# Kernel tuning notes

Measured on AMD Instinct MI355X. Metric: run time of the kernel, lower is better.

The kernel has to match this reference:

```python
import jax, jax.numpy as jnp
import numpy as np

L, D, H, FF = 4, 512, 8, 1024
B, S = 8, 480
TPT = 15          # TOKENS_PER_TURN
FIELD_IDX = 0
CAP = 6.0         # tanh logit soft cap
NEG = -1e30


def _layer_norm(x, g, b, eps=1e-5):
    m = jnp.mean(x, axis=-1, keepdims=True)
    v = jnp.mean((x - m) ** 2, axis=-1, keepdims=True)
    return (x - m) * jax.lax.rsqrt(v + eps) * g + b


def _episodic_mask(expanded_ids, n_prev_fields):
    # pokemon_batched_episodic_mask, vectorized -> [B, S, S] bool
    idx = jnp.arange(S)
    q_t = (idx // TPT)[:, None]            # [S,1]
    kv_t = (idx // TPT)[None, :]           # [1,S]
    kv_i = (idx % TPT)[None, :]
    same_turn = q_t == kv_t
    prev_field = (kv_i == FIELD_IDX) & (kv_t < q_t) & (q_t - kv_t <= n_prev_fields)
    same_ep = expanded_ids[:, :, None] == expanded_ids[:, None, :]  # [B,S,S]
    return same_ep & (same_turn | prev_field)[None]


def setup_inputs() -> dict:
    key = jax.random.key(0)
    ks = jax.random.split(key, 6)
    x = jax.random.normal(ks[0], (B, S, D), dtype=jnp.float32)
    expanded_ids = jnp.sort(jax.random.randint(ks[1], (B, S), 0, 3), axis=-1)
    inp = {
        "x": x,
        "expanded_ids": expanded_ids,
        "n_prev_fields": 8,
        "Wqkv": 0.02 * jax.random.normal(ks[2], (L, D, 3 * D), dtype=jnp.float32),
        "bqkv": jnp.zeros((L, 3 * D), jnp.float32),
        "Wo": 0.02 * jax.random.normal(ks[3], (L, D, D), dtype=jnp.float32),
        "bo": jnp.zeros((L, D), jnp.float32),
        "g1": jnp.ones((L, D), jnp.float32),
        "b1": jnp.zeros((L, D), jnp.float32),
        "g2": jnp.ones((L, D), jnp.float32),
        "b2": jnp.zeros((L, D), jnp.float32),
        "W1": 0.02 * jax.random.normal(ks[4], (L, D, FF), dtype=jnp.float32),
        "bf1": jnp.zeros((L, FF), jnp.float32),
        "W2": 0.02 * jax.random.normal(ks[5], (L, FF, D), dtype=jnp.float32),
        "bf2": jnp.zeros((L, D), jnp.float32),
    }
    return inp


def _encoder_layer(x, mask, Wqkv, bqkv, Wo, bo, g1, b1, g2, b2, W1, bf1, W2, bf2):
    hd = D // H
    h = _layer_norm(x, g1, b1)
    qkv = h @ Wqkv + bqkv                               # [B,S,3D]
    qkv = qkv.reshape(B, S, 3, H, hd)
    q, k, v = (qkv[:, :, i].transpose(0, 2, 1, 3) for i in range(3))  # [B,H,S,hd]
    scores = jnp.einsum("bhqd,bhkd->bhqk", q, k) / jnp.sqrt(jnp.float32(hd))
    scores = CAP * jnp.tanh(scores / CAP)               # logit soft cap (score_mod)
    scores = jnp.where(mask[:, None], scores, NEG)      # episodic block mask
    attn = jax.nn.softmax(scores, axis=-1)
    out = jnp.einsum("bhqk,bhkd->bhqd", attn, v)
    out = out.transpose(0, 2, 1, 3).reshape(B, S, D)
    x = x + (out @ Wo + bo)
    h2 = _layer_norm(x, g2, b2)
    ff = jax.nn.gelu(h2 @ W1 + bf1, approximate=False) @ W2 + bf2
    return x + ff


def reference(x, expanded_ids, n_prev_fields, Wqkv, bqkv, Wo, bo, g1, b1, g2, b2, W1, bf1, W2, bf2):
    mask = _episodic_mask(expanded_ids, n_prev_fields)
    for l in range(L):
        x = _encoder_layer(x, mask, Wqkv[l], bqkv[l], Wo[l], bo[l],
                           g1[l], b1[l], g2[l], b2[l], W1[l], bf1[l], W2[l], bf2[l])
    return x
```

## Files before the change

kernel.cpp:

```cpp
#include <hip/hip_runtime.h>
#include <hip/hip_bf16.h>
#include <hip/hip_fp16.h>
#include <math.h>

#define NL 4
#define Dm 512
#define Hh 8
#define FFD 1024
#define Bb 8
#define Ss 480
#define TPT 15
#define ROWS (Bb*Ss)

typedef __attribute__((ext_vector_type(8))) short short8v;
typedef __attribute__((ext_vector_type(4))) float f32x4;
typedef __attribute__((ext_vector_type(2))) _Float16 half2v;
typedef __attribute__((ext_vector_type(8))) _Float16 half8v;

#if __has_builtin(__builtin_amdgcn_fdot2)
#define FDOT2(a, b, c) __builtin_amdgcn_fdot2(a, b, c, false)
#else
#define FDOT2(a, b, c) ((c) + (float)(a)[0] * (float)(b)[0] + (float)(a)[1] * (float)(b)[1])
#endif

__device__ __forceinline__ void gld_lds16(const void* g, void* lbase, int lane) {
#if __has_builtin(__builtin_amdgcn_global_load_lds)
    __builtin_amdgcn_global_load_lds((const __attribute__((address_space(1))) void*)g,
                                     (__attribute__((address_space(3))) void*)lbase, 16, 0, 0);
#else
    *(short8v*)((char*)lbase + lane * 16) = *(const short8v*)g;
#endif
}

__global__ __launch_bounds__(256) void ln_kernel(const float* __restrict__ x,
                                                 const float* __restrict__ g,
                                                 const float* __restrict__ b,
                                                 __hip_bfloat16* __restrict__ out) {
    int row = blockIdx.x;
    const float* xr = x + (size_t)row * Dm;
    int tid = threadIdx.x;
    int wid = tid >> 6, lane = tid & 63;
    float v0 = xr[tid], v1 = xr[tid + 256];

    __shared__ float red[8];
    float s = v0 + v1;
    for (int off = 32; off; off >>= 1) s += __shfl_down(s, off);
    if (lane == 0) red[wid] = s;
    __syncthreads();
    if (tid == 0) red[0] = (red[0] + red[1] + red[2] + red[3]) * (1.0f / Dm);
    __syncthreads();
    float mean = red[0];

    float d0 = v0 - mean, d1 = v1 - mean;
    float ss = d0 * d0 + d1 * d1;
    for (int off = 32; off; off >>= 1) ss += __shfl_down(ss, off);
    if (lane == 0) red[4 + wid] = ss;
    __syncthreads();
    if (tid == 0) red[4] = (red[4] + red[5] + red[6] + red[7]) * (1.0f / Dm);
    __syncthreads();
    float rstd = rsqrtf(red[4] + 1e-5f);

    out[(size_t)row * Dm + tid]       = __float2bfloat16(d0 * rstd * g[tid]       + b[tid]);
    out[(size_t)row * Dm + tid + 256] = __float2bfloat16(d1 * rstd * g[tid + 256] + b[tid + 256]);
}

__global__ __launch_bounds__(256) void conv_t_kernel(const float* __restrict__ in,
                                                     __hip_bfloat16* __restrict__ out,
                                                     int K, int N) {
    const float* inz = in + (size_t)blockIdx.z * K * N;
    __hip_bfloat16* outz = out + (size_t)blockIdx.z * K * N;
    __shared__ float t[32][33];
    int n0 = blockIdx.x * 32, k0 = blockIdx.y * 32;
    int tx = threadIdx.x & 31, ty = threadIdx.x >> 5;
#pragma unroll
    for (int r = 0; r < 4; r++)
        t[ty * 4 + r][tx] = inz[(size_t)(k0 + ty * 4 + r) * N + n0 + tx];
    __syncthreads();
#pragma unroll
    for (int r = 0; r < 4; r++)
        outz[(size_t)(n0 + ty * 4 + r) * K + k0 + tx] = __float2bfloat16(t[tx][ty * 4 + r]);
}

template <int ACT, int RES, int OUTMODE>
__global__ __launch_bounds__(256) void gemm_mfma(const __hip_bfloat16* __restrict__ A,
                                                 const __hip_bfloat16* __restrict__ Bt,
                                                 const float* __restrict__ bias,
                                                 const float* __restrict__ res,
                                                 void* __restrict__ C,
                                                 int M, int N, int K) {
    __shared__ __align__(16) short As[64 * 64];
    __shared__ __align__(16) short Bs[64 * 64];
    const int bm = blockIdx.y * 64, bn = blockIdx.x * 64;
    const int tid = threadIdx.x;
    const int w = tid >> 6, lane = tid & 63;
    const int wm = (w >> 1) * 32, wn = (w & 1) * 32;
    const int l16 = lane & 15, lq = lane >> 4;
    const short* Ag = (const short*)A;
    const short* Bg = (const short*)Bt;

    f32x4 acc[2][2] = {};

    for (int k0 = 0; k0 < K; k0 += 64) {
#pragma unroll
        for (int r = 0; r < 2; ++r) {
            int row = r * 32 + w * 8 + (lane >> 3);
            int csrc = (lane & 7) ^ (row & 7);
            void* la = &As[(size_t)(r * 4096 + w * 1024) / 2];
            void* lb = &Bs[(size_t)(r * 4096 + w * 1024) / 2];
            gld_lds16(Ag + (size_t)(bm + row) * K + k0 + csrc * 8, la, lane);
            gld_lds16(Bg + (size_t)(bn + row) * K + k0 + csrc * 8, lb, lane);
        }
        __syncthreads();
#pragma unroll
        for (int kc = 0; kc < 2; ++kc) {
            short8v af[2], bf[2];
#pragma unroll
            for (int i = 0; i < 2; i++) {
                int row = wm + i * 16 + l16;
                int ch = (kc * 4 + lq) ^ (row & 7);
                af[i] = *(const short8v*)(&As[row * 64 + ch * 8]);
                int col = wn + i * 16 + l16;
                int ch2 = (kc * 4 + lq) ^ (col & 7);
                bf[i] = *(const short8v*)(&Bs[col * 64 + ch2 * 8]);
            }
#pragma unroll
            for (int i = 0; i < 2; i++)
#pragma unroll
                for (int j = 0; j < 2; j++)
                    acc[i][j] = __builtin_amdgcn_mfma_f32_16x16x32_bf16(
                        af[i], bf[j], acc[i][j], 0, 0, 0);
        }
        __syncthreads();
    }

#pragma unroll
    for (int i = 0; i < 2; i++) {
#pragma unroll
        for (int j = 0; j < 2; j++) {
#pragma unroll
            for (int r = 0; r < 4; r++) {
                int mrow = bm + wm + i * 16 + lq * 4 + r;
                int ncol = bn + wn + j * 16 + l16;
                float v = acc[i][j][r] + bias[ncol];
                if (ACT == 1) v = 0.5f * v * (1.0f + erff(v * 0.70710678118f));
                if (RES) v += res[(size_t)mrow * N + ncol];
                if (OUTMODE == 0)      ((float*)C)[(size_t)mrow * N + ncol] = v;
                else if (OUTMODE == 1) ((__hip_bfloat16*)C)[(size_t)mrow * N + ncol] = __float2bfloat16(v);
                else                   ((__half*)C)[(size_t)mrow * N + ncol] = __float2half(v);
            }
        }
    }
}

__global__ __launch_bounds__(256) void attn_sparse(const _Float16* __restrict__ qkv,
                                                   const int* __restrict__ ids,
                                                   const int* __restrict__ npf_p,
                                                   __hip_bfloat16* __restrict__ outb) {
    __shared__ _Float16 qs[4][512];
    __shared__ float ps[4][Hh][24];
    int w = threadIdx.x >> 6, lane = threadIdx.x & 63;
    int bq = blockIdx.x * 4 + w;
    int q = bq % Ss, b = bq / Ss;
    int npf = npf_p[0];
    int qt = q / TPT;
    int qid = ids[bq];

    *(half8v*)&qs[w][lane * 8] = *(const half8v*)&qkv[(size_t)bq * 1536 + lane * 8];
    __syncthreads();

    int h = lane >> 3, cp = lane & 7;

    half2v qreg[32];
#pragma unroll
    for (int i = 0; i < 32; i++) qreg[i] = *(const half2v*)&qs[w][h * 64 + i * 2];

    float s[3];
#pragma unroll
    for (int i = 0; i < 3; i++) {
        int c = cp + i * 8;
        float sv = -INFINITY;
        if (c < 23) {
            bool ok; int k;
            if (c < 15) { k = qt * TPT + c; ok = true; }
            else { int dt = c - 14; int kt = qt - dt; k = kt * TPT; ok = (kt >= 0) && (dt <= npf); }
            if (ok && ids[b * Ss + k] == qid) {
                const half8v* kr = (const half8v*)&qkv[(size_t)(b * Ss + k) * 1536 + 512 + h * 64];
                float dot = 0.0f;
#pragma unroll
                for (int cch = 0; cch < 8; cch++) {
                    half8v kv = kr[cch];
#pragma unroll
                    for (int e = 0; e < 4; e++) {
                        half2v kk = { kv[e * 2], kv[e * 2 + 1] };
                        dot = FDOT2(qreg[cch * 4 + e], kk, dot);
                    }
                }
                sv = 6.0f * tanhf(dot * (0.125f / 6.0f));
            }
        }
        s[i] = sv;
    }

    float m = fmaxf(fmaxf(s[0], s[1]), s[2]);
    for (int off = 1; off < 8; off <<= 1) m = fmaxf(m, __shfl_xor(m, off));
    float p0 = expf(s[0] - m), p1 = expf(s[1] - m), p2 = expf(s[2] - m);
    float l = p0 + p1 + p2;
    for (int off = 1; off < 8; off <<= 1) l += __shfl_xor(l, off);
    float inv = 1.0f / l;
    if (cp < 8)       ps[w][h][cp]      = p0 * inv;
    if (cp + 8 < 23)  ps[w][h][cp + 8]  = p1 * inv;
    if (cp + 16 < 23) ps[w][h][cp + 16] = p2 * inv;
    __syncthreads();

    int dg = lane & 7;
    float o[8] = {};
    for (int c = 0; c < 23; c++) {
        float p = ps[w][h][c];
        if (p != 0.0f) {
            int k = (c < 15) ? (qt * TPT + c) : ((qt - (c - 14)) * TPT);
            half8v vv = *(const half8v*)&qkv[(size_t)(b * Ss + k) * 1536 + 1024 + h * 64 + dg * 8];
#pragma unroll
            for (int e = 0; e < 8; e++) o[e] += p * (float)vv[e];
        }
    }
    short8v pack;
#pragma unroll
    for (int e = 0; e < 8; e++) {
        __hip_bfloat16 t = __float2bfloat16(o[e]);
        pack[e] = __builtin_bit_cast(short, t);
    }
    *(short8v*)&outb[(size_t)bq * Dm + h * 64 + dg * 8] = pack;
}

extern "C" void kernel_launch(void* const* d_in, const int* in_sizes, int n_in,
                              void* d_out, int out_size, void* d_ws, size_t ws_size,
                              hipStream_t stream) {
    const float* x    = (const float*)d_in[0];
    const int*   ids  = (const int*)d_in[1];
    const int*   npf  = (const int*)d_in[2];
    const float* Wqkv = (const float*)d_in[3];
    const float* bqkv = (const float*)d_in[4];
    const float* Wo   = (const float*)d_in[5];
    const float* bo   = (const float*)d_in[6];
    const float* g1   = (const float*)d_in[7];
    const float* b1   = (const float*)d_in[8];
    const float* g2   = (const float*)d_in[9];
    const float* b2   = (const float*)d_in[10];
    const float* W1   = (const float*)d_in[11];
    const float* bf1  = (const float*)d_in[12];
    const float* W2   = (const float*)d_in[13];
    const float* bf2  = (const float*)d_in[14];
    float* out = (float*)d_out;

    char* p = (char*)d_ws;
    __hip_bfloat16* hb    = (__hip_bfloat16*)p;   p += (size_t)ROWS * Dm * 2;
    _Float16*       qkvb  = (_Float16*)p;         p += (size_t)ROWS * 3 * Dm * 2;
    __hip_bfloat16* attnb = (__hip_bfloat16*)p;   p += (size_t)ROWS * Dm * 2;
    __hip_bfloat16* fb    = (__hip_bfloat16*)p;   p += (size_t)ROWS * FFD * 2;
    __hip_bfloat16* Wqkv_t= (__hip_bfloat16*)p;   p += (size_t)NL * Dm * 3 * Dm * 2;
    __hip_bfloat16* Wo_t  = (__hip_bfloat16*)p;   p += (size_t)NL * Dm * Dm * 2;
    __hip_bfloat16* W1_t  = (__hip_bfloat16*)p;   p += (size_t)NL * Dm * FFD * 2;
    __hip_bfloat16* W2_t  = (__hip_bfloat16*)p;   p += (size_t)NL * FFD * Dm * 2;

    conv_t_kernel<<<dim3(3 * Dm / 32, Dm / 32, NL), 256, 0, stream>>>(Wqkv, Wqkv_t, Dm, 3 * Dm);
    conv_t_kernel<<<dim3(Dm / 32, Dm / 32, NL),     256, 0, stream>>>(Wo,   Wo_t,   Dm, Dm);
    conv_t_kernel<<<dim3(FFD / 32, Dm / 32, NL),    256, 0, stream>>>(W1,   W1_t,   Dm, FFD);
    conv_t_kernel<<<dim3(Dm / 32, FFD / 32, NL),    256, 0, stream>>>(W2,   W2_t,   FFD, Dm);

    for (int l = 0; l < NL; l++) {
        const float* xin = (l == 0) ? x : out;
        ln_kernel<<<ROWS, 256, 0, stream>>>(xin, g1 + l * Dm, b1 + l * Dm, hb);
        gemm_mfma<0, 0, 2><<<dim3(24, 60), 256, 0, stream>>>(
            hb, Wqkv_t + (size_t)l * Dm * 3 * Dm, bqkv + l * 3 * Dm, nullptr, qkvb,
            ROWS, 3 * Dm, Dm);
        attn_sparse<<<ROWS / 4, 256, 0, stream>>>(qkvb, ids, npf, attnb);
        gemm_mfma<0, 1, 0><<<dim3(8, 60), 256, 0, stream>>>(
            attnb, Wo_t + (size_t)l * Dm * Dm, bo + l * Dm, xin, out,
            ROWS, Dm, Dm);
        ln_kernel<<<ROWS, 256, 0, stream>>>(out, g2 + l * Dm, b2 + l * Dm, hb);
        gemm_mfma<1, 0, 1><<<dim3(16, 60), 256, 0, stream>>>(
            hb, W1_t + (size_t)l * Dm * FFD, bf1 + l * FFD, nullptr, fb,
            ROWS, FFD, Dm);
        gemm_mfma<0, 1, 0><<<dim3(8, 60), 256, 0, stream>>>(
            fb, W2_t + (size_t)l * FFD * Dm, bf2 + l * Dm, out, out,
            ROWS, Dm, FFD);
    }
}
```

Measured before the change: 346.9 us.

## Double-buffer GEMM LDS, add 128-row tiles, warp-per-row layernorm, merge weight conversion

The GEMM kernel now double-buffers its LDS tiles, so the global loads for the next K step are issued before computing on the current one. It also takes a BM template parameter, and the QKV and FFN1 GEMMs use 128-row tiles for more reuse per block. LayerNorm now gives one wavefront per row with vectorized float4 loads and shuffle-only reductions, removing the shared-memory barriers. The four weight transpose/convert launches are merged into one. The costs are more LDS per block, which may lower occupancy, and fewer blocks for the 128-row GEMMs.

```diff
diff --git a/kernel.cpp b/kernel.cpp
--- a/kernel.cpp
+++ b/kernel.cpp
@@ -36,105 +36,147 @@
                                                  const float* __restrict__ g,
                                                  const float* __restrict__ b,
                                                  __hip_bfloat16* __restrict__ out) {
-    int row = blockIdx.x;
-    const float* xr = x + (size_t)row * Dm;
-    int tid = threadIdx.x;
-    int wid = tid >> 6, lane = tid & 63;
-    float v0 = xr[tid], v1 = xr[tid + 256];
-
-    __shared__ float red[8];
-    float s = v0 + v1;
-    for (int off = 32; off; off >>= 1) s += __shfl_down(s, off);
-    if (lane == 0) red[wid] = s;
+    int w = threadIdx.x >> 6, lane = threadIdx.x & 63;
+    int row = blockIdx.x * 4 + w;
+    const float* xr = x + (size_t)row * Dm + lane * 8;
+    float4 v0 = *(const float4*)xr;
+    float4 v1 = *(const float4*)(xr + 4);
+    float v[8] = { v0.x, v0.y, v0.z, v0.w, v1.x, v1.y, v1.z, v1.w };
+
+    float s = 0.0f;
+#pragma unroll
+    for (int e = 0; e < 8; e++) s += v[e];
+#pragma unroll
+    for (int off = 1; off < 64; off <<= 1) s += __shfl_xor(s, off);
+    float mean = s * (1.0f / Dm);
+
+    float ss = 0.0f;
+#pragma unroll
+    for (int e = 0; e < 8; e++) { v[e] -= mean; ss += v[e] * v[e]; }
+#pragma unroll
+    for (int off = 1; off < 64; off <<= 1) ss += __shfl_xor(ss, off);
+    float rstd = rsqrtf(ss * (1.0f / Dm) + 1e-5f);
+
+    const float* gp = g + lane * 8;
+    const float* bp = b + lane * 8;
+    float4 g0 = *(const float4*)gp, g1 = *(const float4*)(gp + 4);
+    float4 b0 = *(const float4*)bp, b1 = *(const float4*)(bp + 4);
+    float gg[8] = { g0.x, g0.y, g0.z, g0.w, g1.x, g1.y, g1.z, g1.w };
+    float bb[8] = { b0.x, b0.y, b0.z, b0.w, b1.x, b1.y, b1.z, b1.w };
+    short8v pack;
+#pragma unroll
+    for (int e = 0; e < 8; e++) {
+        __hip_bfloat16 t = __float2bfloat16(v[e] * rstd * gg[e] + bb[e]);
+        pack[e] = __builtin_bit_cast(short, t);
+    }
+    *(short8v*)&out[(size_t)row * Dm + lane * 8] = pack;
+}
+
+__global__ __launch_bounds__(256) void conv_all(const float* __restrict__ Wqkv,
+                                                const float* __restrict__ Wo,
+                                                const float* __restrict__ W1,
+                                                const float* __restrict__ W2,
+                                                __hip_bfloat16* __restrict__ oq,
+                                                __hip_bfloat16* __restrict__ oo,
+                                                __hip_bfloat16* __restrict__ o1,
+                                                __hip_bfloat16* __restrict__ o2) {
+    int type = blockIdx.z >> 2, l = blockIdx.z & 3;
+    int K, N; const float* src; __hip_bfloat16* dst;
+    if (type == 0)      { K = 512;  N = 1536; src = Wqkv; dst = oq; }
+    else if (type == 1) { K = 512;  N = 512;  src = Wo;   dst = oo; }
+    else if (type == 2) { K = 512;  N = 1024; src = W1;   dst = o1; }
+    else                { K = 1024; N = 512;  src = W2;   dst = o2; }
+    int n0 = blockIdx.x * 32, k0 = blockIdx.y * 32;
+    if (n0 >= N || k0 >= K) return;
+    src += (size_t)l * K * N;
+    dst += (size_t)l * K * N;
+
+    __shared__ float t[32][33];
+    int tx = threadIdx.x & 31, ty = threadIdx.x >> 5;
+#pragma unroll
+    for (int r = 0; r < 4; r++)
+        t[ty * 4 + r][tx] = src[(size_t)(k0 + ty * 4 + r) * N + n0 + tx];
     __syncthreads();
-    if (tid == 0) red[0] = (red[0] + red[1] + red[2] + red[3]) * (1.0f / Dm);
-    __syncthreads();
-    float mean = red[0];
-
-    float d0 = v0 - mean, d1 = v1 - mean;
-    float ss = d0 * d0 + d1 * d1;
-    for (int off = 32; off; off >>= 1) ss += __shfl_down(ss, off);
-    if (lane == 0) red[4 + wid] = ss;
-    __syncthreads();
-    if (tid == 0) red[4] = (red[4] + red[5] + red[6] + red[7]) * (1.0f / Dm);
-    __syncthreads();
-    float rstd = rsqrtf(red[4] + 1e-5f);
-
-    out[(size_t)row * Dm + tid]       = __float2bfloat16(d0 * rstd * g[tid]       + b[tid]);
-    out[(size_t)row * Dm + tid + 256] = __float2bfloat16(d1 * rstd * g[tid + 256] + b[tid + 256]);
-}
-
-__global__ __launch_bounds__(256) void conv_t_kernel(const float* __restrict__ in,
-                                                     __hip_bfloat16* __restrict__ out,
-                                                     int K, int N) {
-    const float* inz = in + (size_t)blockIdx.z * K * N;
-    __hip_bfloat16* outz = out + (size_t)blockIdx.z * K * N;
-    __shared__ float t[32][33];
-    int n0 = blockIdx.x * 32, k0 = blockIdx.y * 32;
-    int tx = threadIdx.x & 31, ty = threadIdx.x >> 5;
 #pragma unroll
     for (int r = 0; r < 4; r++)
-        t[ty * 4 + r][tx] = inz[(size_t)(k0 + ty * 4 + r) * N + n0 + tx];
-    __syncthreads();
-#pragma unroll
-    for (int r = 0; r < 4; r++)
-        outz[(size_t)(n0 + ty * 4 + r) * K + k0 + tx] = __float2bfloat16(t[tx][ty * 4 + r]);
-}
-
-template <int ACT, int RES, int OUTMODE>
+        dst[(size_t)(n0 + ty * 4 + r) * K + k0 + tx] = __float2bfloat16(t[tx][ty * 4 + r]);
+}
+
+template <int BM, int ACT, int RES, int OUTMODE>
 __global__ __launch_bounds__(256) void gemm_mfma(const __hip_bfloat16* __restrict__ A,
                                                  const __hip_bfloat16* __restrict__ Bt,
                                                  const float* __restrict__ bias,
                                                  const float* __restrict__ res,
                                                  void* __restrict__ C,
                                                  int M, int N, int K) {
-    __shared__ __align__(16) short As[64 * 64];
-    __shared__ __align__(16) short Bs[64 * 64];
-    const int bm = blockIdx.y * 64, bn = blockIdx.x * 64;
+    constexpr int MF = BM / 32;
+    constexpr int AC = BM / 32;
+    __shared__ __align__(16) short As[2][BM * 64];
+    __shared__ __align__(16) short Bs[2][64 * 64];
+    const int bm = blockIdx.y * BM, bn = blockIdx.x * 64;
     const int tid = threadIdx.x;
     const int w = tid >> 6, lane = tid & 63;
-    const int wm = (w >> 1) * 32, wn = (w & 1) * 32;
+    const int wm = (w >> 1) * (BM / 2), wn = (w & 1) * 32;
     const int l16 = lane & 15, lq = lane >> 4;
     const short* Ag = (const short*)A;
     const short* Bg = (const short*)Bt;
-
-    f32x4 acc[2][2] = {};
-
-    for (int k0 = 0; k0 < K; k0 += 64) {
-#pragma unroll
-        for (int r = 0; r < 2; ++r) {
-            int row = r * 32 + w * 8 + (lane >> 3);
-            int csrc = (lane & 7) ^ (row & 7);
-            void* la = &As[(size_t)(r * 4096 + w * 1024) / 2];
-            void* lb = &Bs[(size_t)(r * 4096 + w * 1024) / 2];
-            gld_lds16(Ag + (size_t)(bm + row) * K + k0 + csrc * 8, la, lane);
-            gld_lds16(Bg + (size_t)(bn + row) * K + k0 + csrc * 8, lb, lane);
-        }
-        __syncthreads();
+    const int nt = K >> 6;
+
+    f32x4 acc[MF][2] = {};
+
+    auto stage = [&](int t, int buf) {
+        int k0 = t << 6;
+#pragma unroll
+        for (int c = 0; c < AC; ++c) {
+            int e = c * 256 + tid;
+            int row = e >> 3;
+            int csrc = (e & 7) ^ (row & 7);
+            gld_lds16(Ag + (size_t)(bm + row) * K + k0 + csrc * 8,
+                      &As[buf][(c * 256 + w * 64) * 8], lane);
+        }
+#pragma unroll
+        for (int c = 0; c < 2; ++c) {
+            int e = c * 256 + tid;
+            int row = e >> 3;
+            int csrc = (e & 7) ^ (row & 7);
+            gld_lds16(Bg + (size_t)(bn + row) * K + k0 + csrc * 8,
+                      &Bs[buf][(c * 256 + w * 64) * 8], lane);
+        }
+    };
+
+    stage(0, 0);
+    __syncthreads();
+    int cur = 0;
+    for (int t = 0; t < nt; ++t) {
+        if (t + 1 < nt) stage(t + 1, cur ^ 1);
 #pragma unroll
         for (int kc = 0; kc < 2; ++kc) {
-            short8v af[2], bf[2];
-#pragma unroll
-            for (int i = 0; i < 2; i++) {
+            short8v af[MF], bf[2];
+#pragma unroll
+            for (int i = 0; i < MF; i++) {
                 int row = wm + i * 16 + l16;
                 int ch = (kc * 4 + lq) ^ (row & 7);
-                af[i] = *(const short8v*)(&As[row * 64 + ch * 8]);
-                int col = wn + i * 16 + l16;
+                af[i] = *(const short8v*)(&As[cur][row * 64 + ch * 8]);
+            }
+#pragma unroll
+            for (int j = 0; j < 2; j++) {
+                int col = wn + j * 16 + l16;
                 int ch2 = (kc * 4 + lq) ^ (col & 7);
-                bf[i] = *(const short8v*)(&Bs[col * 64 + ch2 * 8]);
+                bf[j] = *(const short8v*)(&Bs[cur][col * 64 + ch2 * 8]);
             }
 #pragma unroll
-            for (int i = 0; i < 2; i++)
+            for (int i = 0; i < MF; i++)
 #pragma unroll
                 for (int j = 0; j < 2; j++)
                     acc[i][j] = __builtin_amdgcn_mfma_f32_16x16x32_bf16(
                         af[i], bf[j], acc[i][j], 0, 0, 0);
         }
         __syncthreads();
-    }
-
-#pragma unroll
-    for (int i = 0; i < 2; i++) {
+        cur ^= 1;
+    }
+
+#pragma unroll
+    for (int i = 0; i < MF; i++) {
 #pragma unroll
         for (int j = 0; j < 2; j++) {
 #pragma unroll
@@ -262,26 +304,24 @@
     __hip_bfloat16* W1_t  = (__hip_bfloat16*)p;   p += (size_t)NL * Dm * FFD * 2;
     __hip_bfloat16* W2_t  = (__hip_bfloat16*)p;   p += (size_t)NL * FFD * Dm * 2;
 
-    conv_t_kernel<<<dim3(3 * Dm / 32, Dm / 32, NL), 256, 0, stream>>>(Wqkv, Wqkv_t, Dm, 3 * Dm);
-    conv_t_kernel<<<dim3(Dm / 32, Dm / 32, NL),     256, 0, stream>>>(Wo,   Wo_t,   Dm, Dm);
-    conv_t_kernel<<<dim3(FFD / 32, Dm / 32, NL),    256, 0, stream>>>(W1,   W1_t,   Dm, FFD);
-    conv_t_kernel<<<dim3(Dm / 32, FFD / 32, NL),    256, 0, stream>>>(W2,   W2_t,   FFD, Dm);
+    conv_all<<<dim3(48, 32, 16), 256, 0, stream>>>(Wqkv, Wo, W1, W2,
+                                                   Wqkv_t, Wo_t, W1_t, W2_t);
 
     for (int l = 0; l < NL; l++) {
         const float* xin = (l == 0) ? x : out;
-        ln_kernel<<<ROWS, 256, 0, stream>>>(xin, g1 + l * Dm, b1 + l * Dm, hb);
-        gemm_mfma<0, 0, 2><<<dim3(24, 60), 256, 0, stream>>>(
+        ln_kernel<<<ROWS / 4, 256, 0, stream>>>(xin, g1 + l * Dm, b1 + l * Dm, hb);
+        gemm_mfma<128, 0, 0, 2><<<dim3(24, 30), 256, 0, stream>>>(
             hb, Wqkv_t + (size_t)l * Dm * 3 * Dm, bqkv + l * 3 * Dm, nullptr, qkvb,
             ROWS, 3 * Dm, Dm);
         attn_sparse<<<ROWS / 4, 256, 0, stream>>>(qkvb, ids, npf, attnb);
-        gemm_mfma<0, 1, 0><<<dim3(8, 60), 256, 0, stream>>>(
+        gemm_mfma<64, 0, 1, 0><<<dim3(8, 60), 256, 0, stream>>>(
             attnb, Wo_t + (size_t)l * Dm * Dm, bo + l * Dm, xin, out,
             ROWS, Dm, Dm);
-        ln_kernel<<<ROWS, 256, 0, stream>>>(out, g2 + l * Dm, b2 + l * Dm, hb);
-        gemm_mfma<1, 0, 1><<<dim3(16, 60), 256, 0, stream>>>(
+        ln_kernel<<<ROWS / 4, 256, 0, stream>>>(out, g2 + l * Dm, b2 + l * Dm, hb);
+        gemm_mfma<128, 1, 0, 1><<<dim3(16, 30), 256, 0, stream>>>(
             hb, W1_t + (size_t)l * Dm * FFD, bf1 + l * FFD, nullptr, fb,
             ROWS, FFD, Dm);
-        gemm_mfma<0, 1, 0><<<dim3(8, 60), 256, 0, stream>>>(
+        gemm_mfma<64, 0, 1, 0><<<dim3(8, 60), 256, 0, stream>>>(
             fb, W2_t + (size_t)l * FFD * Dm, bf2 + l * Dm, out, out,
             ROWS, Dm, FFD);
     }
```

Measured after the change: 322.6 us. -7.0%, faster.
